# Kernel tuning notes

Measured on AMD Instinct MI355X. Metric: run time of the kernel, lower is better.

The kernel has to match this reference:

```python
import jax, jax.numpy as jnp
import numpy as np

N, NH, D, REP, C, SUB = 512, 32, 1024, 1024, 16, 64
GAMA, EPS, LN_EPS = 0.9, 1e-10, 1e-5
IMG_H, IMG_W = 800, 1280


def spatial_enc(b1, b2, h, w):
    # pocket.ops.compute_spatial_encodings: 18 handcrafted pair features + their logs -> 36
    c1x = (b1[:, 0] + b1[:, 2]) * 0.5; c1y = (b1[:, 1] + b1[:, 3]) * 0.5
    c2x = (b2[:, 0] + b2[:, 2]) * 0.5; c2y = (b2[:, 1] + b2[:, 3]) * 0.5
    b1w = b1[:, 2] - b1[:, 0]; b1h = b1[:, 3] - b1[:, 1]
    b2w = b2[:, 2] - b2[:, 0]; b2h = b2[:, 3] - b2[:, 1]
    dx = jnp.abs(c2x - c1x) / (b1w + EPS)
    dy = jnp.abs(c2y - c1y) / (b1h + EPS)
    ltx = jnp.maximum(b1[:, 0], b2[:, 0]); lty = jnp.maximum(b1[:, 1], b2[:, 1])
    rbx = jnp.minimum(b1[:, 2], b2[:, 2]); rby = jnp.minimum(b1[:, 3], b2[:, 3])
    inter = jnp.clip(rbx - ltx, 0.0) * jnp.clip(rby - lty, 0.0)
    a1 = b1w * b1h; a2 = b2w * b2h
    iou = inter / (a1 + a2 - inter)
    f = jnp.stack([
        c1x / w, c1y / h, c2x / w, c2y / h,
        b1w / w, b1h / h, b2w / w, b2h / h,
        a1 / (h * w), a2 / (h * w), a2 / (a1 + EPS),
        b1w / (b1h + EPS), b2w / (b2h + EPS), iou,
        (c2x > c1x) * dx, (c2x < c1x) * dx,
        (c2y > c1y) * dy, (c2y < c1y) * dy,
    ], axis=1)
    return jnp.concatenate([f, jnp.log(f + EPS)], axis=1)


def mbf(a, s, w1, b1, w2, b2, w3, b3):
    # relu(sum_c fc3_c(relu(fc1_c(a) * fc2_c(s)))) with branches batched over c
    u1 = jnp.einsum('pd,cdk->cpk', a, w1) + b1[:, None, :]
    u2 = jnp.einsum('ps,csk->cpk', s, w2) + b2[:, None, :]
    hdn = jax.nn.relu(u1 * u2)  # [C,P,SUB]
    out = jnp.einsum('cpk,cko->po', hdn, w3) + b3.sum(0)
    return jax.nn.relu(out)


def ln(x, g, b):
    m = x.mean(-1, keepdims=True)
    v = ((x - m) ** 2).mean(-1, keepdims=True)
    return (x - m) / jnp.sqrt(v + LN_EPS) * g + b


def setup_inputs():
    key = jax.random.key(0)
    ks = jax.random.split(key, 16)
    labels = jnp.where(jnp.arange(N) < NH, 0, 1).astype(jnp.int32)  # first NH nodes are humans
    node = jax.random.normal(ks[0], (N, D), jnp.float32)
    cx = jax.random.uniform(ks[1], (N,)) * (IMG_W * 0.5)
    cy = jax.random.uniform(ks[2], (N,)) * (IMG_H * 0.5)
    bw = jax.random.uniform(ks[3], (N,)) * (IMG_W * 0.3) + 8.0
    bh = jax.random.uniform(ks[4], (N,)) * (IMG_H * 0.3) + 8.0
    coords = jnp.stack([cx, cy, cx + bw, cy + bh], axis=1)
    p = lambda k, shp: jax.random.normal(k, shp, jnp.float32) * 0.02
    return dict(
        labels=labels, node=node, coords=coords, image_h=IMG_H, image_w=IMG_W,
        sp_w1=p(ks[5], (36, 128)), sp_b1=jnp.zeros(128),
        sp_w2=p(ks[6], (128, 256)), sp_b2=jnp.zeros(256),
        sp_w3=p(ks[7], (256, 1024)), sp_b3=jnp.zeros(1024),
        att_w1=p(ks[8], (C, 2 * D, SUB)), att_b1=jnp.zeros((C, SUB)),
        att_w2=p(ks[9], (C, 1024, SUB)), att_b2=jnp.zeros((C, SUB)),
        att_w3=p(ks[10], (C, SUB, REP)), att_b3=jnp.zeros((C, REP)),
        adj_w=p(ks[11], (REP,)), adj_b=jnp.zeros(()),
        lnh_g=jnp.ones(D), lnh_b=jnp.zeros(D),
        lno_g=jnp.ones(D), lno_b=jnp.zeros(D),
    )


def reference(labels, node, coords, image_h, image_w,
              sp_w1, sp_b1, sp_w2, sp_b2, sp_w3, sp_b3,
              att_w1, att_b1, att_w2, att_b2, att_w3, att_b3,
              adj_w, adj_b, lnh_g, lnh_b, lno_g, lno_b):
    n = node.shape[0]
    n_h = int((np.asarray(labels) == 0).sum())
    xi = np.repeat(np.arange(n_h), n)  # human index per pair
    yj = np.tile(np.arange(n), n_h)    # node index per pair
    keep = np.nonzero(xi != yj)[0]
    x = jnp.asarray(xi); y = jnp.asarray(yj)
    x_keep = jnp.asarray(xi[keep]); y_keep = jnp.asarray(yj[keep])

    f = spatial_enc(coords[x], coords[y], float(image_h), float(image_w))  # [P,36]
    sp = jax.nn.relu(f @ sp_w1 + sp_b1)
    sp = jax.nn.relu(sp @ sp_w2 + sp_b2)
    sp = jax.nn.relu(sp @ sp_w3 + sp_b3)  # [P,1024]

    human_node = node[:n_h]
    adjacency = None
    for _ in range(2):  # num_iter
        a = jnp.concatenate([human_node[x], node[y]], axis=1)  # [P,2D]
        weight = mbf(a, sp, att_w1, att_b1, att_w2, att_b2, att_w3, att_b3)  # [P,REP]
        adjacency = jax.nn.relu(weight @ adj_w + adj_b).reshape(n_h, n)
        hn_msg = adjacency @ node          # einsum('yx,xa->ya', adj, node)
        nd_msg = adjacency.T @ human_node  # einsum('yx,xa->ya', adj.T, human)
        node = ln(node * GAMA + (1.0 - GAMA) * nd_msg, lno_g, lno_b)
        human_node = ln(human_node * GAMA + (1.0 - GAMA) * hn_msg, lnh_g, lnh_b)

    return (human_node[x_keep], node[y_keep], adjacency[x_keep, y_keep], x_keep, y_keep)
```

## Files before the change

### kernel.cpp

```cpp
#include <hip/hip_runtime.h>
#include <hip/hip_bf16.h>


typedef __attribute__((ext_vector_type(4))) float  f32x4;
typedef __attribute__((ext_vector_type(8))) __bf16 bf16x8;
typedef __attribute__((ext_vector_type(4))) __bf16 bf16x4;

#define FEPS 1e-10f
#define LNEPS 1e-5f
#define GAMA_F 0.9f

__device__ __forceinline__ void gload16(const void* g, void* l) {
  __builtin_amdgcn_global_load_lds(
      (const __attribute__((address_space(1))) void*)g,
      (__attribute__((address_space(3))) void*)l, 16, 0, 0);
}

__device__ __forceinline__ float read_dim(const void* p) {
  int iv = *(const int*)p;
  if (iv > 0 && iv < (1 << 20)) return (float)iv;
  return *(const float*)p;
}

__global__ void prep_mega(const float* __restrict__ w1, const float* __restrict__ w2,
                          const float* __restrict__ w3, const float* __restrict__ spw3,
                          const float* __restrict__ spw1, const float* __restrict__ spw2,
                          const float* __restrict__ b3,
                          const float* __restrict__ node_in,
                          const float* __restrict__ coords,
                          const void* __restrict__ imh, const void* __restrict__ imw,
                          __bf16* __restrict__ W1at, __bf16* __restrict__ W1bt,
                          __bf16* __restrict__ W2t, __bf16* __restrict__ W3t,
                          __bf16* __restrict__ SpW3t,
                          __bf16* __restrict__ SpW1t, __bf16* __restrict__ SpW2t,
                          float* __restrict__ b3s,
                          float* __restrict__ node_f, __bf16* __restrict__ node_b,
                          float* __restrict__ hn_f, __bf16* __restrict__ hn_b,
                          __bf16* __restrict__ f36) {
  __shared__ float tile[64][65];
  const int b = blockIdx.x, t = threadIdx.x;
  const int tc = t & 63, tr = t >> 6;
  if (b < 256) {
    const int c = b >> 4, d0 = (b & 15) << 6;
    #pragma unroll
    for (int pass = 0; pass < 2; ++pass) {
      const float* src = w1 + (size_t)c * 131072 + (size_t)(d0 + pass * 1024) * 64;
      __bf16* dst = pass ? W1bt : W1at;
      if (pass) __syncthreads();
      #pragma unroll
      for (int q = 0; q < 16; ++q) {
        int dd = q * 4 + tr;
        tile[dd][tc] = src[dd * 64 + tc];
      }
      __syncthreads();
      #pragma unroll
      for (int q = 0; q < 16; ++q) {
        int kk = q * 4 + tr;
        dst[(size_t)(c * 64 + kk) * 1024 + d0 + tc] = (__bf16)tile[tc][kk];
      }
    }
  } else if (b < 512) {
    const int bb = b - 256, c = bb >> 4, s0 = (bb & 15) << 6;
    const float* src = w2 + (size_t)c * 65536 + (size_t)s0 * 64;
    #pragma unroll
    for (int q = 0; q < 16; ++q) {
      int ss = q * 4 + tr;
      tile[ss][tc] = src[ss * 64 + tc];
    }
    __syncthreads();
    #pragma unroll
    for (int q = 0; q < 16; ++q) {
      int kk = q * 4 + tr;
      W2t[(size_t)(c * 64 + kk) * 1024 + s0 + tc] = (__bf16)tile[tc][kk];
    }
  } else if (b < 768) {
    const int bb = b - 512, c = bb >> 4, o0 = (bb & 15) << 6;
    const float* src = w3 + (size_t)c * 65536;
    #pragma unroll
    for (int q = 0; q < 16; ++q) {
      int kk = q * 4 + tr;
      tile[kk][tc] = src[kk * 1024 + o0 + tc];
    }
    __syncthreads();
    #pragma unroll
    for (int q = 0; q < 16; ++q) {
      int oo = q * 4 + tr;
      W3t[(size_t)(o0 + oo) * 1024 + c * 64 + tc] = (__bf16)tile[tc][oo];
    }
  } else if (b < 832) {
    const int bb = b - 768, o0 = (bb >> 2) << 6, k0 = (bb & 3) << 6;
    #pragma unroll
    for (int q = 0; q < 16; ++q) {
      int kk = q * 4 + tr;
      tile[kk][tc] = spw3[(size_t)(k0 + kk) * 1024 + o0 + tc];
    }
    __syncthreads();
    #pragma unroll
    for (int q = 0; q < 16; ++q) {
      int oo = q * 4 + tr;
      SpW3t[(size_t)(o0 + oo) * 256 + k0 + tc] = (__bf16)tile[tc][oo];
    }
  } else if (b < 960) {
    int gid = (b - 832) * 256 + t;
    if (gid < 8192) {
      int n = gid >> 6, k = gid & 63;
      SpW1t[gid] = (k < 36) ? (__bf16)spw1[k * 128 + n] : (__bf16)0.f;
    }
    {
      int n = gid >> 7, k = gid & 127;
      SpW2t[gid] = (__bf16)spw2[k * 256 + n];
    }
    if (gid < 1024) {
      float s = 0.f;
      for (int cc = 0; cc < 16; ++cc) s += b3[cc * 1024 + gid];
      b3s[gid] = s;
    }
  } else if (b < 3008) {
    int gid = (b - 960) * 256 + t;
    float v = node_in[gid];
    node_f[gid] = v;
    node_b[gid] = (__bf16)v;
    if (gid < 32 * 1024) { hn_f[gid] = v; hn_b[gid] = (__bf16)v; }
  } else {
    int p = (b - 3008) * 256 + t;
    int i = p >> 9, j = p & 511;
    float H = read_dim(imh), W = read_dim(imw);
    f32x4 b1 = ((const f32x4*)coords)[i];
    f32x4 b2 = ((const f32x4*)coords)[j];
    float c1x = (b1[0] + b1[2]) * 0.5f, c1y = (b1[1] + b1[3]) * 0.5f;
    float c2x = (b2[0] + b2[2]) * 0.5f, c2y = (b2[1] + b2[3]) * 0.5f;
    float b1w = b1[2] - b1[0], b1h = b1[3] - b1[1];
    float b2w = b2[2] - b2[0], b2h = b2[3] - b2[1];
    float dx = fabsf(c2x - c1x) / (b1w + FEPS);
    float dy = fabsf(c2y - c1y) / (b1h + FEPS);
    float ltx = fmaxf(b1[0], b2[0]), lty = fmaxf(b1[1], b2[1]);
    float rbx = fminf(b1[2], b2[2]), rby = fminf(b1[3], b2[3]);
    float inter = fmaxf(rbx - ltx, 0.f) * fmaxf(rby - lty, 0.f);
    float a1 = b1w * b1h, a2 = b2w * b2h;
    float iou = inter / (a1 + a2 - inter);
    float f[18];
    f[0] = c1x / W;  f[1] = c1y / H;  f[2] = c2x / W;  f[3] = c2y / H;
    f[4] = b1w / W;  f[5] = b1h / H;  f[6] = b2w / W;  f[7] = b2h / H;
    f[8] = a1 / (H * W); f[9] = a2 / (H * W); f[10] = a2 / (a1 + FEPS);
    f[11] = b1w / (b1h + FEPS); f[12] = b2w / (b2h + FEPS); f[13] = iou;
    f[14] = (c2x > c1x) ? dx : 0.f; f[15] = (c2x < c1x) ? dx : 0.f;
    f[16] = (c2y > c1y) ? dy : 0.f; f[17] = (c2y < c1y) ? dy : 0.f;
    __bf16 o[64];
    #pragma unroll
    for (int q = 0; q < 18; ++q) { o[q] = (__bf16)f[q]; o[18 + q] = (__bf16)logf(f[q] + FEPS); }
    #pragma unroll
    for (int q = 36; q < 64; ++q) o[q] = (__bf16)0.f;
    bf16x8* dst = (bf16x8*)(f36 + (size_t)p * 64);
    #pragma unroll
    for (int q = 0; q < 8; ++q) dst[q] = *(bf16x8*)&o[q * 8];
  }
}

__global__ __launch_bounds__(256)
void mlp_head(const __bf16* __restrict__ f36, const __bf16* __restrict__ SpW1t,
              const __bf16* __restrict__ SpW2t, const float* __restrict__ b1,
              const float* __restrict__ b2, __bf16* __restrict__ sp2out) {
  __shared__ __align__(16) __bf16 Af[64 * 64];
  __shared__ __align__(16) __bf16 S1[64 * 128];
  const int t = threadIdx.x;
  const int lane = t & 63, wv = t >> 6;
  const int wr = wv >> 1, wc = wv & 1;
  const int lr = lane & 15, lg = lane >> 4;
  const int m0 = blockIdx.x * 64;

  gload16(f36 + (size_t)m0 * 64 + t * 16, &Af[t * 16]);
  gload16(f36 + (size_t)m0 * 64 + 4096 + t * 8, &Af[4096 + t * 8]);
  __syncthreads();

  {
    f32x4 acc[2][4] = {};
    #pragma unroll
    for (int ks = 0; ks < 2; ++ks) {
      bf16x8 af[2], bf[4];
      #pragma unroll
      for (int mi = 0; mi < 2; ++mi)
        af[mi] = *(const bf16x8*)&Af[(wr * 32 + mi * 16 + lr) * 64 + ks * 32 + lg * 8];
      #pragma unroll
      for (int ni = 0; ni < 4; ++ni)
        bf[ni] = *(const bf16x8*)(SpW1t + (size_t)(wc * 64 + ni * 16 + lr) * 64 + ks * 32 + lg * 8);
      #pragma unroll
      for (int mi = 0; mi < 2; ++mi)
        #pragma unroll
        for (int ni = 0; ni < 4; ++ni)
          acc[mi][ni] = __builtin_amdgcn_mfma_f32_16x16x32_bf16(af[mi], bf[ni], acc[mi][ni], 0, 0, 0);
    }
    #pragma unroll
    for (int mi = 0; mi < 2; ++mi)
      #pragma unroll
      for (int r = 0; r < 4; ++r) {
        int R = wr * 32 + mi * 16 + lg * 4 + r;
        #pragma unroll
        for (int ni = 0; ni < 4; ++ni) {
          int Cc = wc * 64 + ni * 16 + lr;
          S1[R * 128 + Cc] = (__bf16)fmaxf(acc[mi][ni][r] + b1[Cc], 0.f);
        }
      }
  }
  __syncthreads();

  {
    f32x4 acc[2][8] = {};
    #pragma unroll
    for (int ks = 0; ks < 4; ++ks) {
      bf16x8 af[2];
      #pragma unroll
      for (int mi = 0; mi < 2; ++mi)
        af[mi] = *(const bf16x8*)&S1[(wr * 32 + mi * 16 + lr) * 128 + ks * 32 + lg * 8];
      #pragma unroll
      for (int ni = 0; ni < 8; ++ni) {
        bf16x8 bf = *(const bf16x8*)(SpW2t + (size_t)(wc * 128 + ni * 16 + lr) * 128 + ks * 32 + lg * 8);
        #pragma unroll
        for (int mi = 0; mi < 2; ++mi)
          acc[mi][ni] = __builtin_amdgcn_mfma_f32_16x16x32_bf16(af[mi], bf, acc[mi][ni], 0, 0, 0);
      }
    }
    #pragma unroll
    for (int mi = 0; mi < 2; ++mi)
      #pragma unroll
      for (int r = 0; r < 4; ++r) {
        int R = m0 + wr * 32 + mi * 16 + lg * 4 + r;
        #pragma unroll
        for (int ni = 0; ni < 8; ++ni) {
          int Cc = wc * 128 + ni * 16 + lr;
          sp2out[(size_t)R * 256 + Cc] = (__bf16)fmaxf(acc[mi][ni][r] + b2[Cc], 0.f);
        }
      }
  }
}

template <int EPI>
__global__ __launch_bounds__(256)
void gemm_bt(const __bf16* __restrict__ A, const __bf16* __restrict__ Bt,
             const float* __restrict__ bias, void* __restrict__ C,
             int N, int K) {
  __shared__ __align__(16) __bf16 As[128 * 64];
  __shared__ __align__(16) __bf16 Bs[128 * 64];
  const int t = threadIdx.x;
  const int lane = t & 63, wv = t >> 6;
  const int wr = wv >> 1, wc = wv & 1;
  const int lr = lane & 15, lg = lane >> 4;
  const int lrow = lane >> 3, lcol = (lane & 7) << 3;
  const int b = blockIdx.x;
  const int xcd = b & 7, seq = b >> 3;
  const int m0 = (xcd * 16 + (seq >> 3)) * 128;
  const int n0 = (seq & 7) * 128;

  f32x4 acc[4][4] = {};
  const int nkt = K >> 6;
  for (int kt = 0; kt < nkt; ++kt) {
    const int k0 = kt << 6;
    #pragma unroll
    for (int it = 0; it < 4; ++it) {
      const int rbase = wv * 32 + it * 8;
      gload16(A + (size_t)(m0 + rbase + lrow) * K + k0 + lcol, &As[rbase * 64]);
      gload16(Bt + (size_t)(n0 + rbase + lrow) * K + k0 + lcol, &Bs[rbase * 64]);
    }
    __syncthreads();
    #pragma unroll
    for (int ks = 0; ks < 2; ++ks) {
      bf16x8 af[4], bfr[4];
      #pragma unroll
      for (int mi = 0; mi < 4; ++mi)
        af[mi] = *(const bf16x8*)&As[(wr * 64 + mi * 16 + lr) * 64 + ks * 32 + lg * 8];
      #pragma unroll
      for (int ni = 0; ni < 4; ++ni)
        bfr[ni] = *(const bf16x8*)&Bs[(wc * 64 + ni * 16 + lr) * 64 + ks * 32 + lg * 8];
      #pragma unroll
      for (int mi = 0; mi < 4; ++mi)
        #pragma unroll
        for (int ni = 0; ni < 4; ++ni)
          acc[mi][ni] = __builtin_amdgcn_mfma_f32_16x16x32_bf16(af[mi], bfr[ni], acc[mi][ni], 0, 0, 0);
    }
    __syncthreads();
  }
  #pragma unroll
  for (int mi = 0; mi < 4; ++mi)
    #pragma unroll
    for (int r = 0; r < 4; ++r) {
      int R = m0 + wr * 64 + mi * 16 + lg * 4 + r;
      #pragma unroll
      for (int ni = 0; ni < 4; ++ni) {
        int Cc = n0 + wc * 64 + ni * 16 + lr;
        float v = acc[mi][ni][r] + bias[Cc];
        if constexpr (EPI == 0) v = fmaxf(v, 0.f);
        ((__bf16*)C)[(size_t)R * N + Cc] = (__bf16)v;
      }
    }
}

__global__ __launch_bounds__(256)
void gemm_u1(const __bf16* __restrict__ hn_b, const __bf16* __restrict__ node_b,
             const __bf16* __restrict__ W1at, const __bf16* __restrict__ W1bt,
             const float* __restrict__ b1, float* __restrict__ H1, float* __restrict__ N1) {
  __shared__ __align__(16) __bf16 As[32 * 64];
  __shared__ __align__(16) __bf16 Bs[128 * 64];
  const int t = threadIdx.x;
  const int lane = t & 63, wv = t >> 6;
  const int wr = wv >> 1, wc = wv & 1;
  const int lr = lane & 15, lg = lane >> 4;
  const int lrow = lane >> 3, lcol = (lane & 7) << 3;
  const bool isH = (blockIdx.x == 0);
  const __bf16* Ap = isH ? hn_b : node_b + (size_t)(blockIdx.x - 1) * 32 * 1024;
  const __bf16* Bp = isH ? W1at : W1bt;
  const int n0 = blockIdx.y * 128;

  f32x4 acc[4] = {};
  for (int kt = 0; kt < 16; ++kt) {
    const int k0 = kt << 6;
    gload16(Ap + (size_t)(wv * 8 + lrow) * 1024 + k0 + lcol, &As[(wv * 8) * 64]);
    #pragma unroll
    for (int it = 0; it < 4; ++it) {
      const int rbase = wv * 32 + it * 8;
      gload16(Bp + (size_t)(n0 + rbase + lrow) * 1024 + k0 + lcol, &Bs[rbase * 64]);
    }
    __syncthreads();
    #pragma unroll
    for (int ks = 0; ks < 2; ++ks) {
      bf16x8 af = *(const bf16x8*)&As[(wr * 16 + lr) * 64 + ks * 32 + lg * 8];
      #pragma unroll
      for (int ni = 0; ni < 4; ++ni) {
        bf16x8 bfr = *(const bf16x8*)&Bs[(wc * 64 + ni * 16 + lr) * 64 + ks * 32 + lg * 8];
        acc[ni] = __builtin_amdgcn_mfma_f32_16x16x32_bf16(af, bfr, acc[ni], 0, 0, 0);
      }
    }
    __syncthreads();
  }
  #pragma unroll
  for (int ni = 0; ni < 4; ++ni)
    #pragma unroll
    for (int r = 0; r < 4; ++r) {
      int R = wr * 16 + lg * 4 + r;
      int Cc = n0 + wc * 64 + ni * 16 + lr;
      float v = acc[ni][r];
      if (isH) H1[(size_t)R * 1024 + Cc] = v + b1[Cc];
      else     N1[((size_t)(blockIdx.x - 1) * 32 + R) * 1024 + Cc] = v;
    }
}

__global__ void build_hdn(const __bf16* __restrict__ u2, const float* __restrict__ H1,
                          const float* __restrict__ N1, __bf16* __restrict__ hdn) {
  int gid = blockIdx.x * 256 + threadIdx.x;
  int p = gid >> 7, c8 = (gid & 127) << 3;
  int i = p >> 9, j = p & 511;
  bf16x8 u = *(const bf16x8*)(u2 + (size_t)p * 1024 + c8);
  const float* hp = H1 + (size_t)i * 1024 + c8;
  const float* np = N1 + (size_t)j * 1024 + c8;
  f32x4 h0 = *(const f32x4*)hp, h1 = *(const f32x4*)(hp + 4);
  f32x4 n0 = *(const f32x4*)np, n1 = *(const f32x4*)(np + 4);
  bf16x8 o;
  #pragma unroll
  for (int e = 0; e < 4; ++e) {
    o[e]     = (__bf16)fmaxf((h0[e] + n0[e]) * (float)u[e], 0.f);
    o[4 + e] = (__bf16)fmaxf((h1[e] + n1[e]) * (float)u[4 + e], 0.f);
  }
  *(bf16x8*)(hdn + (size_t)p * 1024 + c8) = o;
}

__global__ __launch_bounds__(256)
void gemm_adj(const __bf16* __restrict__ hdn, const __bf16* __restrict__ W3t,
              const float* __restrict__ b3s, const float* __restrict__ adjw,
              float* __restrict__ adjpre8) {
  __shared__ __align__(16) __bf16 As[128 * 64];
  __shared__ __align__(16) __bf16 Bs[128 * 64];
  __shared__ float redbuf[2][128];
  const int t = threadIdx.x;
  const int lane = t & 63, wv = t >> 6;
  const int wr = wv >> 1, wc = wv & 1;
  const int lr = lane & 15, lg = lane >> 4;
  const int lrow = lane >> 3, lcol = (lane & 7) << 3;
  const int b = blockIdx.x;
  const int xcd = b & 7, seq = b >> 3;
  const int m0 = (xcd * 16 + (seq >> 3)) * 128;
  const int h = seq & 7, c0 = h * 128;

  f32x4 acc[4][4] = {};
  for (int kt = 0; kt < 16; ++kt) {
    const int k0 = kt << 6;
    #pragma unroll
    for (int it = 0; it < 4; ++it) {
      const int rbase = wv * 32 + it * 8;
      gload16(hdn + (size_t)(m0 + rbase + lrow) * 1024 + k0 + lcol, &As[rbase * 64]);
      gload16(W3t + (size_t)(c0 + rbase + lrow) * 1024 + k0 + lcol, &Bs[rbase * 64]);
    }
    __syncthreads();
    #pragma unroll
    for (int ks = 0; ks < 2; ++ks) {
      bf16x8 af[4], bfr[4];
      #pragma unroll
      for (int mi = 0; mi < 4; ++mi)
        af[mi] = *(const bf16x8*)&As[(wr * 64 + mi * 16 + lr) * 64 + ks * 32 + lg * 8];
      #pragma unroll
      for (int ni = 0; ni < 4; ++ni)
        bfr[ni] = *(const bf16x8*)&Bs[(wc * 64 + ni * 16 + lr) * 64 + ks * 32 + lg * 8];
      #pragma unroll
      for (int mi = 0; mi < 4; ++mi)
        #pragma unroll
        for (int ni = 0; ni < 4; ++ni)
          acc[mi][ni] = __builtin_amdgcn_mfma_f32_16x16x32_bf16(af[mi], bfr[ni], acc[mi][ni], 0, 0, 0);
    }
    __syncthreads();
  }

  float b3v[4], awv[4];
  #pragma unroll
  for (int ni = 0; ni < 4; ++ni) {
    int Cc = c0 + wc * 64 + ni * 16 + lr;
    b3v[ni] = b3s[Cc];
    awv[ni] = adjw[Cc];
  }
  #pragma unroll
  for (int mi = 0; mi < 4; ++mi)
    #pragma unroll
    for (int r = 0; r < 4; ++r) {
      float s = 0.f;
      #pragma unroll
      for (int ni = 0; ni < 4; ++ni)
        s += fmaxf(acc[mi][ni][r] + b3v[ni], 0.f) * awv[ni];
      s += __shfl_xor(s, 1);
      s += __shfl_xor(s, 2);
      s += __shfl_xor(s, 4);
      s += __shfl_xor(s, 8);
      if (lr == 0)
        redbuf[wc][wr * 64 + mi * 16 + lg * 4 + r] = s;
    }
  __syncthreads();
  if (t < 128)
    adjpre8[(size_t)h * 16384 + m0 + t] = redbuf[0][t] + redbuf[1][t];
}

__global__ void msgln(const float* __restrict__ adjpre8, const float* __restrict__ adjb,
                      const float* __restrict__ node_in_f, const float* __restrict__ hn_in_f,
                      const float* __restrict__ lno_g, const float* __restrict__ lno_b,
                      const float* __restrict__ lnh_g, const float* __restrict__ lnh_b,
                      float* __restrict__ node_out_f, float* __restrict__ hn_out_f,
                      __bf16* __restrict__ node_bb, __bf16* __restrict__ hn_bb) {
  __shared__ float adjrow[512];
  __shared__ float sbuf[4];
  const int row = blockIdx.x, t = threadIdx.x;
  const float ab = adjb[0];
  const bool isH = row < 32;
  f32x4 msg = {0.f, 0.f, 0.f, 0.f};
  if (isH) {
    const int i = row;
    float s0 = 0.f, s1 = 0.f;
    #pragma unroll
    for (int h = 0; h < 8; ++h) {
      s0 += adjpre8[(size_t)h * 16384 + i * 512 + t];
      s1 += adjpre8[(size_t)h * 16384 + i * 512 + 256 + t];
    }
    adjrow[t] = fmaxf(s0 + ab, 0.f);
    adjrow[256 + t] = fmaxf(s1 + ab, 0.f);
    __syncthreads();
    for (int j = 0; j < 512; ++j)
      msg += adjrow[j] * ((const f32x4*)node_in_f)[j * 256 + t];
  } else {
    const int j = row - 32;
    int i = t >> 3, hh = t & 7;
    float v = adjpre8[(size_t)hh * 16384 + i * 512 + j];
    v += __shfl_xor(v, 1);
    v += __shfl_xor(v, 2);
    v += __shfl_xor(v, 4);
    if (hh == 0) adjrow[i] = fmaxf(v + ab, 0.f);
    __syncthreads();
    for (int i2 = 0; i2 < 32; ++i2)
      msg += adjrow[i2] * ((const f32x4*)hn_in_f)[i2 * 256 + t];
  }
  const int r = isH ? row : row - 32;
  const float* X = (isH ? hn_in_f : node_in_f) + (size_t)r * 1024;
  const float* g = isH ? lnh_g : lno_g;
  const float* bb = isH ? lnh_b : lno_b;
  float* Xo = (isH ? hn_out_f : node_out_f) + (size_t)r * 1024;
  __bf16* Xb = (isH ? hn_bb : node_bb) + (size_t)r * 1024;

  f32x4 x = ((const f32x4*)X)[t];
  f32x4 y;
  #pragma unroll
  for (int e = 0; e < 4; ++e) y[e] = x[e] * GAMA_F + (1.0f - GAMA_F) * msg[e];
  float s = y[0] + y[1] + y[2] + y[3];
  #pragma unroll
  for (int mm = 32; mm >= 1; mm >>= 1) s += __shfl_xor(s, mm);
  if ((t & 63) == 0) sbuf[t >> 6] = s;
  __syncthreads();
  float mean = (sbuf[0] + sbuf[1] + sbuf[2] + sbuf[3]) * (1.0f / 1024.0f);
  __syncthreads();
  f32x4 d;
  #pragma unroll
  for (int e = 0; e < 4; ++e) d[e] = y[e] - mean;
  float sq = d[0] * d[0] + d[1] * d[1] + d[2] * d[2] + d[3] * d[3];
  #pragma unroll
  for (int mm = 32; mm >= 1; mm >>= 1) sq += __shfl_xor(sq, mm);
  if ((t & 63) == 0) sbuf[t >> 6] = sq;
  __syncthreads();
  float var = (sbuf[0] + sbuf[1] + sbuf[2] + sbuf[3]) * (1.0f / 1024.0f);
  float inv = rsqrtf(var + LNEPS);
  f32x4 gg = ((const f32x4*)g)[t];
  f32x4 bv = ((const f32x4*)bb)[t];
  f32x4 o;
  bf16x4 ob;
  #pragma unroll
  for (int e = 0; e < 4; ++e) { o[e] = d[e] * inv * gg[e] + bv[e]; ob[e] = (__bf16)o[e]; }
  ((f32x4*)Xo)[t] = o;
  *(bf16x4*)(Xb + t * 4) = ob;
}

__global__ void gather_k(const float* __restrict__ hn, const float* __restrict__ node,
                         const float* __restrict__ adjpre8, const float* __restrict__ adjb,
                         float* __restrict__ out) {
  int p = blockIdx.x, t = threadIdx.x;
  int i = p >> 9, j = p & 511;
  if (i == j) return;
  int m = p - (p + 512) / 513;
  float* out0 = out;
  float* out1 = out + (size_t)16352 * 1024;
  float* out2 = out1 + (size_t)16352 * 1024;
  ((f32x4*)out0)[(size_t)m * 256 + t] = ((const f32x4*)hn)[i * 256 + t];
  ((f32x4*)out1)[(size_t)m * 256 + t] = ((const f32x4*)node)[j * 256 + t];
  if (t == 0) {
    float s = adjb[0];
    #pragma unroll
    for (int h = 0; h < 8; ++h) s += adjpre8[(size_t)h * 16384 + p];
    out2[m] = fmaxf(s, 0.f);
    out2[16352 + m] = (float)i;
    out2[2 * 16352 + m] = (float)j;
  }
}

extern "C" void kernel_launch(void* const* d_in, const int* in_sizes, int n_in,
                              void* d_out, int out_size, void* d_ws, size_t ws_size,
                              hipStream_t stream) {
  const float* node_in = (const float*)d_in[1];
  const float* coords  = (const float*)d_in[2];
  const void*  imh     = d_in[3];
  const void*  imw     = d_in[4];
  const float* sp_w1 = (const float*)d_in[5];
  const float* sp_b1 = (const float*)d_in[6];
  const float* sp_w2 = (const float*)d_in[7];
  const float* sp_b2 = (const float*)d_in[8];
  const float* sp_w3 = (const float*)d_in[9];
  const float* sp_b3 = (const float*)d_in[10];
  const float* att_w1 = (const float*)d_in[11];
  const float* att_b1 = (const float*)d_in[12];
  const float* att_w2 = (const float*)d_in[13];
  const float* att_b2 = (const float*)d_in[14];
  const float* att_w3 = (const float*)d_in[15];
  const float* att_b3 = (const float*)d_in[16];
  const float* adj_w  = (const float*)d_in[17];
  const float* adj_b  = (const float*)d_in[18];
  const float* lnh_g  = (const float*)d_in[19];
  const float* lnh_b  = (const float*)d_in[20];
  const float* lno_g  = (const float*)d_in[21];
  const float* lno_b  = (const float*)d_in[22];

  char* w = (char*)d_ws;
  size_t off = 0;
  auto alloc = [&](size_t bytes) -> char* {
    char* p = w + off;
    off += (bytes + 255) & ~(size_t)255;
    return p;
  };
  __bf16* W1at  = (__bf16*)alloc((size_t)1024 * 1024 * 2);
  __bf16* W1bt  = (__bf16*)alloc((size_t)1024 * 1024 * 2);
  __bf16* W2t   = (__bf16*)alloc((size_t)1024 * 1024 * 2);
  __bf16* W3t   = (__bf16*)alloc((size_t)1024 * 1024 * 2);
  __bf16* SpW1t = (__bf16*)alloc(128 * 64 * 2);
  __bf16* SpW2t = (__bf16*)alloc(256 * 128 * 2);
  __bf16* SpW3t = (__bf16*)alloc(1024 * 256 * 2);
  float*  b3s   = (float*)alloc(1024 * 4);
  __bf16* f36   = (__bf16*)alloc((size_t)16384 * 64 * 2);
  __bf16* sp2   = (__bf16*)alloc((size_t)16384 * 256 * 2);
  __bf16* spb   = (__bf16*)alloc((size_t)16384 * 1024 * 2);
  __bf16* u2    = (__bf16*)alloc((size_t)16384 * 1024 * 2);
  float*  H1    = (float*)alloc((size_t)32 * 1024 * 4);
  float*  N1    = (float*)alloc((size_t)512 * 1024 * 4);
  float*  adjpre8 = (float*)alloc((size_t)8 * 16384 * 4);
  float*  node_f0 = (float*)alloc((size_t)512 * 1024 * 4);
  float*  node_f1 = (float*)alloc((size_t)512 * 1024 * 4);
  float*  hn_f0   = (float*)alloc((size_t)32 * 1024 * 4);
  float*  hn_f1   = (float*)alloc((size_t)32 * 1024 * 4);
  __bf16* node_b  = (__bf16*)alloc((size_t)512 * 1024 * 2);
  __bf16* hn_b    = (__bf16*)alloc((size_t)32 * 1024 * 2);
  if (off > ws_size) return;

  prep_mega<<<3072, 256, 0, stream>>>(att_w1, att_w2, att_w3, sp_w3, sp_w1, sp_w2, att_b3,
                                      node_in, coords, imh, imw,
                                      W1at, W1bt, W2t, W3t, SpW3t, SpW1t, SpW2t, b3s,
                                      node_f0, node_b, hn_f0, hn_b, f36);
  mlp_head<<<256, 256, 0, stream>>>(f36, SpW1t, SpW2t, sp_b1, sp_b2, sp2);
  gemm_bt<0><<<1024, 256, 0, stream>>>(sp2, SpW3t, sp_b3, spb, 1024, 256);
  gemm_bt<1><<<1024, 256, 0, stream>>>(spb, W2t, att_b2, u2, 1024, 1024);

  __bf16* hdn = spb;
  gemm_u1<<<dim3(17, 8), 256, 0, stream>>>(hn_b, node_b, W1at, W1bt, att_b1, H1, N1);
  build_hdn<<<8192, 256, 0, stream>>>(u2, H1, N1, hdn);
  gemm_adj<<<1024, 256, 0, stream>>>(hdn, W3t, b3s, adj_w, adjpre8);
  msgln<<<544, 256, 0, stream>>>(adjpre8, adj_b, node_f0, hn_f0,
                                 lno_g, lno_b, lnh_g, lnh_b,
                                 node_f1, hn_f1, node_b, hn_b);
  gemm_u1<<<dim3(17, 8), 256, 0, stream>>>(hn_b, node_b, W1at, W1bt, att_b1, H1, N1);
  build_hdn<<<8192, 256, 0, stream>>>(u2, H1, N1, hdn);
  gemm_adj<<<1024, 256, 0, stream>>>(hdn, W3t, b3s, adj_w, adjpre8);
  msgln<<<544, 256, 0, stream>>>(adjpre8, adj_b, node_f1, hn_f1,
                                 lno_g, lno_b, lnh_g, lnh_b,
                                 node_f0, hn_f0, node_b, hn_b);

  gather_k<<<16384, 256, 0, stream>>>(hn_f0, node_f0, adjpre8, adj_b, (float*)d_out);
}
```

Baseline: 501.4 us.

## Add double-buffered 256x256-tile GEMM for the u2 and adjacency GEMMs

Adds a new 512-thread GEMM kernel with 256x256 output tiles. It double-buffers LDS, issues the next K tile's global-to-LDS loads while the current tile's MFMAs run, and raises wave priority around the MFMA blocks. It replaces the 128x128-tile kernels for the u2 projection and the fused adjacency GEMM, so the adjacency partial sums now come in 4 column slices instead of 8, and msgln and gather_k are updated to match. The goal is more data reuse per tile and load/compute overlap on the large 16384x1024x1024 GEMMs. The trade-off is heavy LDS use (about 132KB), which allows only one block per CU with 256 blocks total. It also fixes the mlp_head LDS load offsets, which left gaps and wrote past the end of the buffer.

After: 470.7 us. 6.1% less time.

```diff
diff --git a/kernel.cpp b/kernel.cpp
--- a/kernel.cpp
+++ b/kernel.cpp
@@ -168,8 +168,8 @@
   const int lr = lane & 15, lg = lane >> 4;
   const int m0 = blockIdx.x * 64;
 
-  gload16(f36 + (size_t)m0 * 64 + t * 16, &Af[t * 16]);
-  gload16(f36 + (size_t)m0 * 64 + 4096 + t * 8, &Af[4096 + t * 8]);
+  gload16(f36 + (size_t)m0 * 64 + t * 8, &Af[t * 8]);
+  gload16(f36 + (size_t)m0 * 64 + 2048 + t * 8, &Af[2048 + t * 8]);
   __syncthreads();
 
   {
@@ -293,6 +293,137 @@
     }
 }
 
+template <int EPI>
+__global__ __launch_bounds__(512, 2)
+void gemm256(const __bf16* __restrict__ A, const __bf16* __restrict__ Bt,
+             const float* __restrict__ bias, void* __restrict__ C,
+             const float* __restrict__ adjw, float* __restrict__ adjpre4,
+             int K) {
+  __shared__ __align__(16) __bf16 As[2][256 * 64];
+  __shared__ __align__(16) __bf16 Bs[2][256 * 64];
+  __shared__ float redbuf[4][256];
+  const int t = threadIdx.x;
+  const int lane = t & 63;
+  const int wv = t >> 6;
+  const int wm = wv >> 2, wn = wv & 3;
+  const int lr = lane & 15, lg = lane >> 4;
+  const int b = blockIdx.x;
+  const int xcd = b & 7, seq = b >> 3;
+  const int m0 = (xcd * 8 + (seq >> 2)) * 256;
+  const int n0 = (seq & 3) * 256;
+  const int srow = t >> 3, scol = (t & 7) * 8;
+
+  f32x4 acc[8][4] = {};
+  const int nkt = K >> 6;
+
+  #pragma unroll
+  for (int c = 0; c < 4; ++c) {
+    gload16(A + (size_t)(m0 + c * 64 + srow) * K + scol, &As[0][(c * 64 + srow) * 64 + scol]);
+    gload16(Bt + (size_t)(n0 + c * 64 + srow) * K + scol, &Bs[0][(c * 64 + srow) * 64 + scol]);
+  }
+  asm volatile("s_waitcnt vmcnt(0)" ::: "memory");
+  __builtin_amdgcn_s_barrier();
+  __builtin_amdgcn_sched_barrier(0);
+
+  int cur = 0;
+  for (int kt = 0; kt < nkt; ++kt) {
+    const int k1 = (kt + 1) << 6;
+    const __bf16* Acur = &As[cur][0];
+    const __bf16* Bcur = &Bs[cur][0];
+    __bf16* Anxt = &As[cur ^ 1][0];
+    __bf16* Bnxt = &Bs[cur ^ 1][0];
+    const bool more = (kt + 1 < nkt);
+    bf16x8 bfr[4][2];
+    #pragma unroll
+    for (int p = 0; p < 4; ++p) {
+      bf16x8 af[2][2];
+      #pragma unroll
+      for (int m = 0; m < 2; ++m) {
+        const int row = wm * 128 + (2 * p + m) * 16 + lr;
+        af[m][0] = *(const bf16x8*)&Acur[row * 64 + lg * 8];
+        af[m][1] = *(const bf16x8*)&Acur[row * 64 + 32 + lg * 8];
+      }
+      if (p == 0) {
+        #pragma unroll
+        for (int n = 0; n < 4; ++n) {
+          const int row = wn * 64 + n * 16 + lr;
+          bfr[n][0] = *(const bf16x8*)&Bcur[row * 64 + lg * 8];
+          bfr[n][1] = *(const bf16x8*)&Bcur[row * 64 + 32 + lg * 8];
+        }
+      }
+      if (more && p < 2) {
+        #pragma unroll
+        for (int cc = 0; cc < 2; ++cc) {
+          const int c = p * 2 + cc;
+          gload16(A + (size_t)(m0 + c * 64 + srow) * K + k1 + scol, &Anxt[(c * 64 + srow) * 64 + scol]);
+          gload16(Bt + (size_t)(n0 + c * 64 + srow) * K + k1 + scol, &Bnxt[(c * 64 + srow) * 64 + scol]);
+        }
+      }
+      __builtin_amdgcn_s_barrier();
+      __builtin_amdgcn_s_setprio(1);
+      #pragma unroll
+      for (int ks = 0; ks < 2; ++ks)
+        #pragma unroll
+        for (int m = 0; m < 2; ++m)
+          #pragma unroll
+          for (int n = 0; n < 4; ++n)
+            acc[2 * p + m][n] = __builtin_amdgcn_mfma_f32_16x16x32_bf16(
+                af[m][ks], bfr[n][ks], acc[2 * p + m][n], 0, 0, 0);
+      __builtin_amdgcn_s_setprio(0);
+      __builtin_amdgcn_s_barrier();
+    }
+    if (more) {
+      asm volatile("s_waitcnt vmcnt(0)" ::: "memory");
+      __builtin_amdgcn_s_barrier();
+      __builtin_amdgcn_sched_barrier(0);
+    }
+    cur ^= 1;
+  }
+
+  if constexpr (EPI == 1) {
+    #pragma unroll
+    for (int mi = 0; mi < 8; ++mi)
+      #pragma unroll
+      for (int r = 0; r < 4; ++r) {
+        const int R = m0 + wm * 128 + mi * 16 + lg * 4 + r;
+        #pragma unroll
+        for (int ni = 0; ni < 4; ++ni) {
+          const int Cc = n0 + wn * 64 + ni * 16 + lr;
+          ((__bf16*)C)[(size_t)R * 1024 + Cc] = (__bf16)(acc[mi][ni][r] + bias[Cc]);
+        }
+      }
+  } else {
+    float b3v[4], awv[4];
+    #pragma unroll
+    for (int ni = 0; ni < 4; ++ni) {
+      const int Cc = n0 + wn * 64 + ni * 16 + lr;
+      b3v[ni] = bias[Cc];
+      awv[ni] = adjw[Cc];
+    }
+    #pragma unroll
+    for (int mi = 0; mi < 8; ++mi)
+      #pragma unroll
+      for (int r = 0; r < 4; ++r) {
+        float s = 0.f;
+        #pragma unroll
+        for (int ni = 0; ni < 4; ++ni)
+          s += fmaxf(acc[mi][ni][r] + b3v[ni], 0.f) * awv[ni];
+        s += __shfl_xor(s, 1);
+        s += __shfl_xor(s, 2);
+        s += __shfl_xor(s, 4);
+        s += __shfl_xor(s, 8);
+        if (lr == 0)
+          redbuf[wn][wm * 128 + mi * 16 + lg * 4 + r] = s;
+      }
+    __syncthreads();
+    if (t < 256) {
+      const int h = seq & 3;
+      adjpre4[(size_t)h * 16384 + m0 + t] =
+          redbuf[0][t] + redbuf[1][t] + redbuf[2][t] + redbuf[3][t];
+    }
+  }
+}
+
 __global__ __launch_bounds__(256)
 void gemm_u1(const __bf16* __restrict__ hn_b, const __bf16* __restrict__ node_b,
              const __bf16* __restrict__ W1at, const __bf16* __restrict__ W1bt,
@@ -361,79 +492,7 @@
   *(bf16x8*)(hdn + (size_t)p * 1024 + c8) = o;
 }
 
-__global__ __launch_bounds__(256)
-void gemm_adj(const __bf16* __restrict__ hdn, const __bf16* __restrict__ W3t,
-              const float* __restrict__ b3s, const float* __restrict__ adjw,
-              float* __restrict__ adjpre8) {
-  __shared__ __align__(16) __bf16 As[128 * 64];
-  __shared__ __align__(16) __bf16 Bs[128 * 64];
-  __shared__ float redbuf[2][128];
-  const int t = threadIdx.x;
-  const int lane = t & 63, wv = t >> 6;
-  const int wr = wv >> 1, wc = wv & 1;
-  const int lr = lane & 15, lg = lane >> 4;
-  const int lrow = lane >> 3, lcol = (lane & 7) << 3;
-  const int b = blockIdx.x;
-  const int xcd = b & 7, seq = b >> 3;
-  const int m0 = (xcd * 16 + (seq >> 3)) * 128;
-  const int h = seq & 7, c0 = h * 128;
-
-  f32x4 acc[4][4] = {};
-  for (int kt = 0; kt < 16; ++kt) {
-    const int k0 = kt << 6;
-    #pragma unroll
-    for (int it = 0; it < 4; ++it) {
-      const int rbase = wv * 32 + it * 8;
-      gload16(hdn + (size_t)(m0 + rbase + lrow) * 1024 + k0 + lcol, &As[rbase * 64]);
-      gload16(W3t + (size_t)(c0 + rbase + lrow) * 1024 + k0 + lcol, &Bs[rbase * 64]);
-    }
-    __syncthreads();
-    #pragma unroll
-    for (int ks = 0; ks < 2; ++ks) {
-      bf16x8 af[4], bfr[4];
-      #pragma unroll
-      for (int mi = 0; mi < 4; ++mi)
-        af[mi] = *(const bf16x8*)&As[(wr * 64 + mi * 16 + lr) * 64 + ks * 32 + lg * 8];
-      #pragma unroll
-      for (int ni = 0; ni < 4; ++ni)
-        bfr[ni] = *(const bf16x8*)&Bs[(wc * 64 + ni * 16 + lr) * 64 + ks * 32 + lg * 8];
-      #pragma unroll
-      for (int mi = 0; mi < 4; ++mi)
-        #pragma unroll
-        for (int ni = 0; ni < 4; ++ni)
-          acc[mi][ni] = __builtin_amdgcn_mfma_f32_16x16x32_bf16(af[mi], bfr[ni], acc[mi][ni], 0, 0, 0);
-    }
-    __syncthreads();
-  }
-
-  float b3v[4], awv[4];
-  #pragma unroll
-  for (int ni = 0; ni < 4; ++ni) {
-    int Cc = c0 + wc * 64 + ni * 16 + lr;
-    b3v[ni] = b3s[Cc];
-    awv[ni] = adjw[Cc];
-  }
-  #pragma unroll
-  for (int mi = 0; mi < 4; ++mi)
-    #pragma unroll
-    for (int r = 0; r < 4; ++r) {
-      float s = 0.f;
-      #pragma unroll
-      for (int ni = 0; ni < 4; ++ni)
-        s += fmaxf(acc[mi][ni][r] + b3v[ni], 0.f) * awv[ni];
-      s += __shfl_xor(s, 1);
-      s += __shfl_xor(s, 2);
-      s += __shfl_xor(s, 4);
-      s += __shfl_xor(s, 8);
-      if (lr == 0)
-        redbuf[wc][wr * 64 + mi * 16 + lg * 4 + r] = s;
-    }
-  __syncthreads();
-  if (t < 128)
-    adjpre8[(size_t)h * 16384 + m0 + t] = redbuf[0][t] + redbuf[1][t];
-}
-
-__global__ void msgln(const float* __restrict__ adjpre8, const float* __restrict__ adjb,
+__global__ void msgln(const float* __restrict__ adjpre4, const float* __restrict__ adjb,
                       const float* __restrict__ node_in_f, const float* __restrict__ hn_in_f,
                       const float* __restrict__ lno_g, const float* __restrict__ lno_b,
                       const float* __restrict__ lnh_g, const float* __restrict__ lnh_b,
@@ -449,9 +508,9 @@
     const int i = row;
     float s0 = 0.f, s1 = 0.f;
     #pragma unroll
-    for (int h = 0; h < 8; ++h) {
-      s0 += adjpre8[(size_t)h * 16384 + i * 512 + t];
-      s1 += adjpre8[(size_t)h * 16384 + i * 512 + 256 + t];
+    for (int h = 0; h < 4; ++h) {
+      s0 += adjpre4[(size_t)h * 16384 + i * 512 + t];
+      s1 += adjpre4[(size_t)h * 16384 + i * 512 + 256 + t];
     }
     adjrow[t] = fmaxf(s0 + ab, 0.f);
     adjrow[256 + t] = fmaxf(s1 + ab, 0.f);
@@ -461,7 +520,7 @@
   } else {
     const int j = row - 32;
     int i = t >> 3, hh = t & 7;
-    float v = adjpre8[(size_t)hh * 16384 + i * 512 + j];
+    float v = (hh < 4) ? adjpre4[(size_t)hh * 16384 + i * 512 + j] : 0.f;
     v += __shfl_xor(v, 1);
     v += __shfl_xor(v, 2);
     v += __shfl_xor(v, 4);
@@ -509,7 +568,7 @@
 }
 
 __global__ void gather_k(const float* __restrict__ hn, const float* __restrict__ node,
-                         const float* __restrict__ adjpre8, const float* __restrict__ adjb,
+                         const float* __restrict__ adjpre4, const float* __restrict__ adjb,
                          float* __restrict__ out) {
   int p = blockIdx.x, t = threadIdx.x;
   int i = p >> 9, j = p & 511;
@@ -523,7 +582,7 @@
   if (t == 0) {
     float s = adjb[0];
     #pragma unroll
-    for (int h = 0; h < 8; ++h) s += adjpre8[(size_t)h * 16384 + p];
+    for (int h = 0; h < 4; ++h) s += adjpre4[(size_t)h * 16384 + p];
     out2[m] = fmaxf(s, 0.f);
     out2[16352 + m] = (float)i;
     out2[2 * 16352 + m] = (float)j;
@@ -577,7 +636,7 @@
   __bf16* u2    = (__bf16*)alloc((size_t)16384 * 1024 * 2);
   float*  H1    = (float*)alloc((size_t)32 * 1024 * 4);
   float*  N1    = (float*)alloc((size_t)512 * 1024 * 4);
-  float*  adjpre8 = (float*)alloc((size_t)8 * 16384 * 4);
+  float*  adjpre4 = (float*)alloc((size_t)4 * 16384 * 4);
   float*  node_f0 = (float*)alloc((size_t)512 * 1024 * 4);
   float*  node_f1 = (float*)alloc((size_t)512 * 1024 * 4);
   float*  hn_f0   = (float*)alloc((size_t)32 * 1024 * 4);
@@ -592,21 +651,21 @@
                                       node_f0, node_b, hn_f0, hn_b, f36);
   mlp_head<<<256, 256, 0, stream>>>(f36, SpW1t, SpW2t, sp_b1, sp_b2, sp2);
   gemm_bt<0><<<1024, 256, 0, stream>>>(sp2, SpW3t, sp_b3, spb, 1024, 256);
-  gemm_bt<1><<<1024, 256, 0, stream>>>(spb, W2t, att_b2, u2, 1024, 1024);
+  gemm256<1><<<256, 512, 0, stream>>>(spb, W2t, att_b2, u2, nullptr, nullptr, 1024);
 
   __bf16* hdn = spb;
   gemm_u1<<<dim3(17, 8), 256, 0, stream>>>(hn_b, node_b, W1at, W1bt, att_b1, H1, N1);
   build_hdn<<<8192, 256, 0, stream>>>(u2, H1, N1, hdn);
-  gemm_adj<<<1024, 256, 0, stream>>>(hdn, W3t, b3s, adj_w, adjpre8);
-  msgln<<<544, 256, 0, stream>>>(adjpre8, adj_b, node_f0, hn_f0,
+  gemm256<4><<<256, 512, 0, stream>>>(hdn, W3t, b3s, nullptr, adj_w, adjpre4, 1024);
+  msgln<<<544, 256, 0, stream>>>(adjpre4, adj_b, node_f0, hn_f0,
                                  lno_g, lno_b, lnh_g, lnh_b,
                                  node_f1, hn_f1, node_b, hn_b);
   gemm_u1<<<dim3(17, 8), 256, 0, stream>>>(hn_b, node_b, W1at, W1bt, att_b1, H1, N1);
   build_hdn<<<8192, 256, 0, stream>>>(u2, H1, N1, hdn);
-  gemm_adj<<<1024, 256, 0, stream>>>(hdn, W3t, b3s, adj_w, adjpre8);
-  msgln<<<544, 256, 0, stream>>>(adjpre8, adj_b, node_f1, hn_f1,
+  gemm256<4><<<256, 512, 0, stream>>>(hdn, W3t, b3s, nullptr, adj_w, adjpre4, 1024);
+  msgln<<<544, 256, 0, stream>>>(adjpre4, adj_b, node_f1, hn_f1,
                                  lno_g, lno_b, lnh_g, lnh_b,
                                  node_f0, hn_f0, node_b, hn_b);
 
-  gather_k<<<16384, 256, 0, stream>>>(hn_f0, node_f0, adjpre8, adj_b, (float*)d_out);
-}
+  gather_k<<<16384, 256, 0, stream>>>(hn_f0, node_f0, adjpre4, adj_b, (float*)d_out);
+}
```
